# Optimization experiments

Measured on AMD Instinct MI355X. Metric: run time of the kernel, lower is better.

The kernel has to match this reference:

```python
import jax, jax.numpy as jnp
import numpy as np

N = 50000      # nodes
E = 500000     # directed edges
F_IN = 112     # node feature dim
G = 256        # number of graphs in batch


def _lin(key, fan_in, fan_out):
    # torch nn.Linear default init: U(-1/sqrt(fan_in), 1/sqrt(fan_in))
    s = 1.0 / np.sqrt(fan_in)
    kw, kb = jax.random.split(key)
    W = jax.random.uniform(kw, (fan_in, fan_out), jnp.float32, -s, s)
    b = jax.random.uniform(kb, (fan_out,), jnp.float32, -s, s)
    return W, b


def setup_inputs() -> dict:
    key = jax.random.key(0)
    ks = jax.random.split(key, 9)
    x = jax.random.normal(ks[0], (N, F_IN), jnp.float32)
    edge_index = jax.random.randint(ks[1], (2, E), 0, N)
    # sorted graph ids, guaranteeing every graph id 0..G-1 appears
    batch = jnp.sort(jnp.concatenate([jnp.arange(G),
                                      jax.random.randint(ks[2], (N - G,), 0, G)]))
    W1, b1 = _lin(ks[3], F_IN, 336)
    W2, b2 = _lin(ks[4], 336, 168)
    Wg, bg = _lin(ks[5], 168, 84)
    Wf, bf = _lin(ks[6], 84, 42)
    Wo, bo = _lin(ks[7], 42, 1)
    return dict(x=x, edge_index=edge_index, batch=batch,
                W1=W1, b1=b1, W2=W2, b2=b2,
                Wg=Wg, bg=bg, Wf=Wf, bf=bf, Wo=Wo, bo=bo)


def _gcn_conv(x, W, b, src, dst, n):
    """PyG GCNConv: add self-loops, symmetric D^-1/2 A D^-1/2 normalization."""
    h = x @ W                                   # [n, out]
    loop = jnp.arange(n, dtype=src.dtype)
    src_f = jnp.concatenate([src, loop])        # [E+n]
    dst_f = jnp.concatenate([dst, loop])
    deg = jax.ops.segment_sum(jnp.ones(src_f.shape[0], jnp.float32), dst_f, n)
    dinv = jnp.where(deg > 0, jax.lax.rsqrt(deg), 0.0)
    norm = dinv[src_f] * dinv[dst_f]            # [E+n]
    out = jax.ops.segment_sum(h[src_f] * norm[:, None], dst_f, n)
    return out + b


def reference(x, edge_index, batch, W1, b1, W2, b2, Wg, bg, Wf, bf, Wo, bo):
    src, dst = edge_index[0], edge_index[1]
    h = jax.nn.relu(_gcn_conv(x, W1, b1, src, dst, N))
    # dropout is identity in eval mode
    h = jax.nn.relu(_gcn_conv(h, W2, b2, src, dst, N))
    g = jax.ops.segment_max(h, batch, G)        # global max pool -> [G, 168]
    g = jax.nn.relu(g @ Wg + bg)
    g = jax.nn.relu(g @ Wf + bf)
    return g @ Wo + bo                           # [G, 1]
```

## Files before the change

### kernel.cpp

```cpp
#include <hip/hip_runtime.h>
#include <hip/hip_fp16.h>

#define N_NODES 50000
#define MPAD    50048
#define N_EDGES 500000
#define F_IN    112
#define K1P     128
#define F1      336
#define K2P     352
#define F2      168
#define NGRAPH  256
#define SCAN_CHUNK 1024
#define SCAN_BLOCKS ((N_NODES + SCAN_CHUNK - 1) / SCAN_CHUNK)

typedef __attribute__((ext_vector_type(8))) _Float16 f16x8;
typedef __attribute__((ext_vector_type(4))) float f32x4;
typedef unsigned short ushort_t;

__device__ __forceinline__ ushort_t f16_bits(float x) {
    __half h = __float2half_rn(x);
    return *(ushort_t*)&h;
}

__global__ void k_zero_int(int* p, int n) {
    int i = blockIdx.x * blockDim.x + threadIdx.x;
    if (i < n) p[i] = 0;
}
__global__ void k_count_deg(const int* __restrict__ dst, int* __restrict__ dcount, int e2) {
    int i = blockIdx.x * blockDim.x + threadIdx.x;
    if (i < e2) {
        int2 d = ((const int2*)dst)[i];
        atomicAdd(&dcount[d.x], 1);
        atomicAdd(&dcount[d.y], 1);
    }
}

#define CVX_BLOCKS  ((N_NODES * (F_IN / 4) + 255) / 256)
#define CVW1_BLOCKS ((384 * K1P + 255) / 256)
#define CVW2_BLOCKS ((192 * K2P + 255) / 256)
#define RNG_BLOCKS  ((N_NODES + 255) / 256)
#define PREP_BLOCKS (CVX_BLOCKS + CVW1_BLOCKS + CVW2_BLOCKS + RNG_BLOCKS)

__global__ __launch_bounds__(256) void k_prep(const float* __restrict__ x,
                                              const float* __restrict__ W1,
                                              const float* __restrict__ W2,
                                              const int* __restrict__ batch,
                                              ushort_t* __restrict__ x16,
                                              ushort_t* __restrict__ w1t,
                                              ushort_t* __restrict__ w2t,
                                              int* __restrict__ r0, int* __restrict__ r1) {
    int bid = blockIdx.x;
    int t = threadIdx.x;
    if (bid < CVX_BLOCKS) {
        int i = bid * 256 + t;
        if (i < N_NODES * (F_IN / 4)) {
            float4 v = ((const float4*)x)[i];
            __half2 h0 = __floats2half2_rn(v.x, v.y);
            __half2 h1 = __floats2half2_rn(v.z, v.w);
            uint2 u; u.x = *(unsigned*)&h0; u.y = *(unsigned*)&h1;
            ((uint2*)x16)[i] = u;
        }
        return;
    }
    bid -= CVX_BLOCKS;
    if (bid < CVW1_BLOCKS) {
        int idx = bid * 256 + t;
        if (idx < 384 * K1P) {
            int n = idx / K1P, k = idx % K1P;
            float v = (n < F1 && k < F_IN) ? W1[k * F1 + n] : 0.0f;
            w1t[idx] = f16_bits(v);
        }
        return;
    }
    bid -= CVW1_BLOCKS;
    if (bid < CVW2_BLOCKS) {
        int idx = bid * 256 + t;
        if (idx < 192 * K2P) {
            int n = idx / K2P, k = idx % K2P;
            float v = (n < F2 && k < F1) ? W2[k * F2 + n] : 0.0f;
            w2t[idx] = f16_bits(v);
        }
        return;
    }
    bid -= CVW2_BLOCKS;
    {
        int v = bid * 256 + t;
        if (v >= N_NODES) return;
        int b = batch[v];
        if (v == 0 || batch[v - 1] != b) r0[b] = v;
        if (v == N_NODES - 1 || batch[v + 1] != b) r1[b] = v + 1;
    }
}

__global__ __launch_bounds__(SCAN_CHUNK) void k_scan1(const int* __restrict__ dcount,
                                                      int* __restrict__ off,
                                                      int* __restrict__ partials,
                                                      float* __restrict__ dinv, int n) {
    __shared__ int s[SCAN_CHUNK];
    int t = threadIdx.x;
    int i = blockIdx.x * SCAN_CHUNK + t;
    int val = (i < n) ? dcount[i] : 0;
    s[t] = val;
    __syncthreads();
    for (int d = 1; d < SCAN_CHUNK; d <<= 1) {
        int x = (t >= d) ? s[t - d] : 0;
        __syncthreads();
        s[t] += x;
        __syncthreads();
    }
    if (i < n) {
        off[i] = s[t] - val;
        dinv[i] = rsqrtf((float)val + 1.0f);
    }
    if (t == SCAN_CHUNK - 1) partials[blockIdx.x] = s[t];
}
__global__ __launch_bounds__(SCAN_CHUNK) void k_scan3(int* __restrict__ off,
                                                      const int* __restrict__ partials, int n) {
    __shared__ int tmp[SCAN_BLOCKS];
    __shared__ int pref[SCAN_BLOCKS];
    int t = threadIdx.x;
    if (t < SCAN_BLOCKS) tmp[t] = partials[t];
    __syncthreads();
    if (t == 0) {
        int run = 0;
        for (int j = 0; j < SCAN_BLOCKS; ++j) { pref[j] = run; run += tmp[j]; }
    }
    __syncthreads();
    int i = blockIdx.x * SCAN_CHUNK + t;
    if (i < n) off[i] += pref[blockIdx.x];
    if (i == n) off[i] = N_EDGES;
}

__global__ void k_scatter(const int* __restrict__ src, const int* __restrict__ dst,
                          const int* __restrict__ off, int* __restrict__ cur,
                          const float* __restrict__ dinv,
                          int2* __restrict__ csr, int e) {
    int i = blockIdx.x * blockDim.x + threadIdx.x;
    if (i >= e) return;
    int s = src[i], d = dst[i];
    int pos = atomicAdd(&cur[d], 1);
    int2 rec;
    rec.x = s;
    rec.y = __float_as_int(dinv[s] * dinv[d]);
    csr[off[d] + pos] = rec;
}

__global__ __launch_bounds__(256) void k_agg1(const ushort_t* __restrict__ X16,
                                              const int* __restrict__ off,
                                              const int2* __restrict__ csr,
                                              const float* __restrict__ dinv,
                                              ushort_t* __restrict__ aX) {
    int w = (blockIdx.x * 256 + threadIdx.x) >> 6;
    int lane = threadIdx.x & 63;
    if (w >= N_NODES / 2) return;
    const int g = lane >> 5, sl = lane & 31;
    const int v = 2 * w + g;
    const bool act = sl < 28;
    int o0A = off[2 * w], oM = off[2 * w + 1], o1B = off[2 * w + 2];
    int o0 = g ? oM : o0A;
    int n  = g ? (o1B - oM) : (oM - o0A);
    int nmax = max(oM - o0A, o1B - oM);
    float di = dinv[v];
    float4 acc = {0, 0, 0, 0};
    if (act) {
        uint2 u = *(const uint2*)(X16 + (long)v * F_IN + sl * 4);
        float2 f0 = __half22float2(*(__half2*)&u.x);
        float2 f1 = __half22float2(*(__half2*)&u.y);
        float s2 = di * di;
        acc.x = f0.x * s2; acc.y = f0.y * s2; acc.z = f1.x * s2; acc.w = f1.y * s2;
    }
    int nm1 = max(n - 1, 0);
    for (int b = 0; b < nmax; b += 8) {
        int2 e[8];
        #pragma unroll
        for (int j = 0; j < 8; ++j) {
            int cidx = min(o0 + min(b + j, nm1), N_EDGES - 1);
            e[j] = csr[cidx];
        }
        uint2 u[8];
        #pragma unroll
        for (int j = 0; j < 8; ++j) {
            bool valid = (b + j) < n;
            int s = valid ? e[j].x : v;
            if (act) u[j] = *(const uint2*)(X16 + (long)s * F_IN + sl * 4);
        }
        #pragma unroll
        for (int j = 0; j < 8; ++j) {
            bool valid = (b + j) < n;
            float c = valid ? __int_as_float(e[j].y) : 0.0f;
            float2 f0 = __half22float2(*(__half2*)&u[j].x);
            float2 f1 = __half22float2(*(__half2*)&u[j].y);
            acc.x += c * f0.x; acc.y += c * f0.y; acc.z += c * f1.x; acc.w += c * f1.y;
        }
    }
    if (sl < 32) {
        uint2 o = {0, 0};
        if (act) {
            __half2 h0 = __floats2half2_rn(acc.x, acc.y);
            __half2 h1 = __floats2half2_rn(acc.z, acc.w);
            o.x = *(unsigned*)&h0; o.y = *(unsigned*)&h1;
        }
        *(uint2*)(aX + (long)v * K1P + sl * 4) = o;
    }
}

template<int KP, int EPI>
__global__ __launch_bounds__(256) void k_gemm_f16(
        const ushort_t* __restrict__ A, const ushort_t* __restrict__ Bt,
        const float* __restrict__ bias,
        ushort_t* __restrict__ C, int M, int Nreal, int CW) {
    __shared__ ushort_t As[128][40];
    __shared__ ushort_t Bs[64][40];
    const int tid = threadIdx.x;
    const int row0 = blockIdx.y * 128;
    const int col0 = blockIdx.x * 64;
    const int w  = tid >> 6, l = tid & 63;
    const int wm = w >> 1, wn = w & 1;
    const int lm = l & 15, lq = l >> 4;

    f32x4 acc[4][2];
    #pragma unroll
    for (int i = 0; i < 4; ++i)
        #pragma unroll
        for (int j = 0; j < 2; ++j) acc[i][j] = (f32x4){0.f, 0.f, 0.f, 0.f};

    const int arow  = tid >> 2;
    const int akoff = (tid & 3) * 8;

    for (int k0 = 0; k0 < KP; k0 += 32) {
        *(int4*)&As[arow][akoff]      = *(const int4*)&A[(long)(row0 + arow) * KP + k0 + akoff];
        *(int4*)&As[arow + 64][akoff] = *(const int4*)&A[(long)(row0 + arow + 64) * KP + k0 + akoff];
        *(int4*)&Bs[arow][akoff]      = *(const int4*)&Bt[(long)(col0 + arow) * KP + k0 + akoff];
        __syncthreads();

        f16x8 af[4], bf[2];
        #pragma unroll
        for (int ms = 0; ms < 4; ++ms)
            af[ms] = *(const f16x8*)&As[wm * 64 + ms * 16 + lm][lq * 8];
        #pragma unroll
        for (int ns = 0; ns < 2; ++ns)
            bf[ns] = *(const f16x8*)&Bs[wn * 32 + ns * 16 + lm][lq * 8];
        #pragma unroll
        for (int ms = 0; ms < 4; ++ms)
            #pragma unroll
            for (int ns = 0; ns < 2; ++ns)
                acc[ms][ns] = __builtin_amdgcn_mfma_f32_16x16x32_f16(af[ms], bf[ns], acc[ms][ns], 0, 0, 0);
        __syncthreads();
    }

    #pragma unroll
    for (int ms = 0; ms < 4; ++ms) {
        int R = row0 + wm * 64 + ms * 16 + lq * 4;
        #pragma unroll
        for (int ns = 0; ns < 2; ++ns) {
            int col = col0 + wn * 32 + ns * 16 + lm;
            if (EPI == 1) {
                if (col < CW) {
                    float bb = (col < Nreal) ? bias[col] : 0.0f;
                    #pragma unroll
                    for (int i = 0; i < 4; ++i) {
                        int row = R + i;
                        if (row < M) {
                            float r = (col < Nreal) ? fmaxf(acc[ms][ns][i] + bb, 0.0f) : 0.0f;
                            C[(long)row * CW + col] = f16_bits(r);
                        }
                    }
                }
            } else {
                if (col < Nreal) {
                    #pragma unroll
                    for (int i = 0; i < 4; ++i) {
                        int row = R + i;
                        if (row < M) C[(long)row * Nreal + col] = f16_bits(acc[ms][ns][i]);
                    }
                }
            }
        }
    }
}

__global__ __launch_bounds__(256) void k_agg2(const ushort_t* __restrict__ T16,
                                              const int* __restrict__ off,
                                              const int2* __restrict__ csr,
                                              const float* __restrict__ dinv,
                                              const float* __restrict__ b2,
                                              ushort_t* __restrict__ out2) {
    int w = (blockIdx.x * 256 + threadIdx.x) >> 6;
    int lane = threadIdx.x & 63;
    if (w >= N_NODES / 2) return;
    const int g = lane >> 5, sl = lane & 31;
    const int v = 2 * w + g;
    const bool act = sl < 21;
    int o0A = off[2 * w], oM = off[2 * w + 1], o1B = off[2 * w + 2];
    int o0 = g ? oM : o0A;
    int n  = g ? (o1B - oM) : (oM - o0A);
    int nmax = max(oM - o0A, o1B - oM);
    float di = dinv[v];
    float4 a0 = {0, 0, 0, 0}, a1 = {0, 0, 0, 0};
    if (act) {
        uint4 u = *(const uint4*)(T16 + (long)v * F2 + sl * 8);
        float2 f0 = __half22float2(*(__half2*)&u.x);
        float2 f1 = __half22float2(*(__half2*)&u.y);
        float2 f2 = __half22float2(*(__half2*)&u.z);
        float2 f3 = __half22float2(*(__half2*)&u.w);
        float s2 = di * di;
        a0.x = f0.x * s2; a0.y = f0.y * s2; a0.z = f1.x * s2; a0.w = f1.y * s2;
        a1.x = f2.x * s2; a1.y = f2.y * s2; a1.z = f3.x * s2; a1.w = f3.y * s2;
    }
    int nm1 = max(n - 1, 0);
    for (int b = 0; b < nmax; b += 8) {
        int2 e[8];
        #pragma unroll
        for (int j = 0; j < 8; ++j) {
            int cidx = min(o0 + min(b + j, nm1), N_EDGES - 1);
            e[j] = csr[cidx];
        }
        uint4 u[8];
        #pragma unroll
        for (int j = 0; j < 8; ++j) {
            bool valid = (b + j) < n;
            int s = valid ? e[j].x : v;
            if (act) u[j] = *(const uint4*)(T16 + (long)s * F2 + sl * 8);
        }
        #pragma unroll
        for (int j = 0; j < 8; ++j) {
            bool valid = (b + j) < n;
            float c = valid ? __int_as_float(e[j].y) : 0.0f;
            float2 f0 = __half22float2(*(__half2*)&u[j].x);
            float2 f1 = __half22float2(*(__half2*)&u[j].y);
            float2 f2 = __half22float2(*(__half2*)&u[j].z);
            float2 f3 = __half22float2(*(__half2*)&u[j].w);
            a0.x += c * f0.x; a0.y += c * f0.y; a0.z += c * f1.x; a0.w += c * f1.y;
            a1.x += c * f2.x; a1.y += c * f2.y; a1.z += c * f3.x; a1.w += c * f3.y;
        }
    }
    if (act) {
        float4 bb0 = ((const float4*)b2)[sl * 2];
        float4 bb1 = ((const float4*)b2)[sl * 2 + 1];
        __half2 h0 = __floats2half2_rn(fmaxf(a0.x + bb0.x, 0.0f), fmaxf(a0.y + bb0.y, 0.0f));
        __half2 h1 = __floats2half2_rn(fmaxf(a0.z + bb0.z, 0.0f), fmaxf(a0.w + bb0.w, 0.0f));
        __half2 h2 = __floats2half2_rn(fmaxf(a1.x + bb1.x, 0.0f), fmaxf(a1.y + bb1.y, 0.0f));
        __half2 h3 = __floats2half2_rn(fmaxf(a1.z + bb1.z, 0.0f), fmaxf(a1.w + bb1.w, 0.0f));
        uint4 o;
        o.x = *(unsigned*)&h0; o.y = *(unsigned*)&h1;
        o.z = *(unsigned*)&h2; o.w = *(unsigned*)&h3;
        *(uint4*)(out2 + (long)v * F2 + sl * 8) = o;
    }
}

__global__ __launch_bounds__(256) void k_pool_head(const ushort_t* __restrict__ out2,
        const int* __restrict__ r0, const int* __restrict__ r1,
        const float* __restrict__ Wg, const float* __restrict__ bg,
        const float* __restrict__ Wf, const float* __restrict__ bf,
        const float* __restrict__ Wo, const float* __restrict__ bo,
        float* __restrict__ out) {
    __shared__ float4 sm[4][F2 / 4];
    __shared__ float s0[F2];
    __shared__ float s1[84];
    __shared__ float s2[42];
    int gi = blockIdx.x;
    int slot = threadIdx.x >> 6, lane = threadIdx.x & 63;
    int a = r0[gi], b = r1[gi];
    if (lane < F2 / 4) {
        float4 mx = {0, 0, 0, 0};
        for (int v = a + slot; v < b; v += 4) {
            uint2 u = ((const uint2*)(out2 + (long)v * F2))[lane];
            float2 f0 = __half22float2(*(__half2*)&u.x);
            float2 f1 = __half22float2(*(__half2*)&u.y);
            mx.x = fmaxf(mx.x, f0.x); mx.y = fmaxf(mx.y, f0.y);
            mx.z = fmaxf(mx.z, f1.x); mx.w = fmaxf(mx.w, f1.y);
        }
        sm[slot][lane] = mx;
    }
    __syncthreads();
    if (slot == 0 && lane < F2 / 4) {
        float4 m0 = sm[0][lane], m1 = sm[1][lane], m2 = sm[2][lane], m3 = sm[3][lane];
        float4 r;
        r.x = fmaxf(fmaxf(m0.x, m1.x), fmaxf(m2.x, m3.x));
        r.y = fmaxf(fmaxf(m0.y, m1.y), fmaxf(m2.y, m3.y));
        r.z = fmaxf(fmaxf(m0.z, m1.z), fmaxf(m2.z, m3.z));
        r.w = fmaxf(fmaxf(m0.w, m1.w), fmaxf(m2.w, m3.w));
        ((float4*)s0)[lane] = r;
    }
    __syncthreads();
    int t = threadIdx.x;
    if (t < 84) {
        float acc = bg[t];
        #pragma unroll 4
        for (int k = 0; k < F2; ++k) acc += s0[k] * Wg[k * 84 + t];
        s1[t] = fmaxf(acc, 0.0f);
    }
    __syncthreads();
    if (t < 42) {
        float acc = bf[t];
        #pragma unroll 4
        for (int k = 0; k < 84; ++k) acc += s1[k] * Wf[k * 42 + t];
        s2[t] = fmaxf(acc, 0.0f);
    }
    __syncthreads();
    if (t == 0) {
        float acc = bo[0];
        for (int k = 0; k < 42; ++k) acc += s2[k] * Wo[k];
        out[gi] = acc;
    }
}

extern "C" void kernel_launch(void* const* d_in, const int* in_sizes, int n_in,
                              void* d_out, int out_size, void* d_ws, size_t ws_size,
                              hipStream_t stream) {
    const float* x   = (const float*)d_in[0];
    const int*   ei  = (const int*)d_in[1];
    const int*   bat = (const int*)d_in[2];
    const float* W1  = (const float*)d_in[3];
    const float* b1  = (const float*)d_in[4];
    const float* W2  = (const float*)d_in[5];
    const float* b2  = (const float*)d_in[6];
    const float* Wg  = (const float*)d_in[7];
    const float* bg  = (const float*)d_in[8];
    const float* Wf  = (const float*)d_in[9];
    const float* bf  = (const float*)d_in[10];
    const float* Wo  = (const float*)d_in[11];
    const float* bo  = (const float*)d_in[12];
    float* out = (float*)d_out;

    char* p = (char*)d_ws;
    float* dinv     = (float*)p; p += 50048 * 4;
    int*   dcount   = (int*)p;   p += 50048 * 4;
    int*   cur      = (int*)p;   p += 50048 * 4;
    int*   off      = (int*)p;   p += 50064 * 4;
    int*   partials = (int*)p;   p += 64 * 4;
    int*   rng0     = (int*)p;   p += 256 * 4;
    int*   rng1     = (int*)p;   p += 256 * 4;
    int2*  csr      = (int2*)p;  p += (long)N_EDGES * 8;
    ushort_t* x16   = (ushort_t*)p; p += (long)N_NODES * F_IN * 2;
    ushort_t* aX    = (ushort_t*)p; p += (long)MPAD * K1P * 2;
    ushort_t* w1t   = (ushort_t*)p; p += (long)384 * K1P * 2;
    ushort_t* w2t   = (ushort_t*)p; p += (long)192 * K2P * 2;
    ushort_t* h1    = (ushort_t*)p; p += (long)MPAD * K2P * 2;
    ushort_t* t16   = (ushort_t*)p; p += (long)N_NODES * F2 * 2;
    ushort_t* o16   = (ushort_t*)p; p += (long)N_NODES * F2 * 2;

    const int* src = ei;
    const int* dst = ei + N_EDGES;
    const int B = 256;

    k_zero_int<<<(2 * 50048 + B - 1) / B, B, 0, stream>>>(dcount, 2 * 50048);
    k_count_deg<<<(N_EDGES / 2 + B - 1) / B, B, 0, stream>>>(dst, dcount, N_EDGES / 2);
    k_prep<<<PREP_BLOCKS, B, 0, stream>>>(x, W1, W2, bat, x16, w1t, w2t, rng0, rng1);
    k_scan1<<<SCAN_BLOCKS, SCAN_CHUNK, 0, stream>>>(dcount, off, partials, dinv, N_NODES);
    k_scan3<<<SCAN_BLOCKS, SCAN_CHUNK, 0, stream>>>(off, partials, N_NODES);
    k_scatter<<<(N_EDGES + B - 1) / B, B, 0, stream>>>(src, dst, off, cur, dinv, csr, N_EDGES);

    k_agg1<<<(N_NODES / 2 * 64) / 256, 256, 0, stream>>>(x16, off, csr, dinv, aX);
    dim3 gg1(6, MPAD / 128);
    k_gemm_f16<K1P, 1><<<gg1, 256, 0, stream>>>(aX, w1t, b1, h1, N_NODES, F1, K2P);

    dim3 gg2(3, MPAD / 128);
    k_gemm_f16<K2P, 2><<<gg2, 256, 0, stream>>>(h1, w2t, nullptr, t16, N_NODES, F2, 0);
    k_agg2<<<(N_NODES / 2 * 64) / 256, 256, 0, stream>>>(t16, off, csr, dinv, b2, o16);

    k_pool_head<<<NGRAPH, 256, 0, stream>>>(o16, rng0, rng1, Wg, bg, Wf, bf, Wo, bo, out);
}
```

Baseline: 299.4 us.

## Retile GEMMs to wide-N tiles, fold degree count into prep, vectorize scatter

The two GEMM kernels move from 128x64 tiles to 64xNT tiles, with NT=128 for layer 1 and NT=192 for layer 2. The second GEMM then reads each A row once over the whole output width instead of three times. The degree-count kernel is merged into the prep kernel as an extra block range, removing one launch. The scatter kernel now handles two edges per thread with int2 loads. The wider tiles use more accumulators per thread, which may reduce occupancy, and the smaller M tile launches more blocks.

```diff
diff --git a/kernel.cpp b/kernel.cpp
--- a/kernel.cpp
+++ b/kernel.cpp
@@ -26,26 +26,21 @@
     int i = blockIdx.x * blockDim.x + threadIdx.x;
     if (i < n) p[i] = 0;
 }
-__global__ void k_count_deg(const int* __restrict__ dst, int* __restrict__ dcount, int e2) {
-    int i = blockIdx.x * blockDim.x + threadIdx.x;
-    if (i < e2) {
-        int2 d = ((const int2*)dst)[i];
-        atomicAdd(&dcount[d.x], 1);
-        atomicAdd(&dcount[d.y], 1);
-    }
-}
 
 #define CVX_BLOCKS  ((N_NODES * (F_IN / 4) + 255) / 256)
+#define CNT_BLOCKS  ((N_EDGES / 2 + 255) / 256)
 #define CVW1_BLOCKS ((384 * K1P + 255) / 256)
 #define CVW2_BLOCKS ((192 * K2P + 255) / 256)
 #define RNG_BLOCKS  ((N_NODES + 255) / 256)
-#define PREP_BLOCKS (CVX_BLOCKS + CVW1_BLOCKS + CVW2_BLOCKS + RNG_BLOCKS)
+#define PREP_BLOCKS (CVX_BLOCKS + CNT_BLOCKS + CVW1_BLOCKS + CVW2_BLOCKS + RNG_BLOCKS)
 
 __global__ __launch_bounds__(256) void k_prep(const float* __restrict__ x,
+                                              const int* __restrict__ dst,
                                               const float* __restrict__ W1,
                                               const float* __restrict__ W2,
                                               const int* __restrict__ batch,
                                               ushort_t* __restrict__ x16,
+                                              int* __restrict__ dcount,
                                               ushort_t* __restrict__ w1t,
                                               ushort_t* __restrict__ w2t,
                                               int* __restrict__ r0, int* __restrict__ r1) {
@@ -63,6 +58,16 @@
         return;
     }
     bid -= CVX_BLOCKS;
+    if (bid < CNT_BLOCKS) {
+        int i = bid * 256 + t;
+        if (i < N_EDGES / 2) {
+            int2 d = ((const int2*)dst)[i];
+            atomicAdd(&dcount[d.x], 1);
+            atomicAdd(&dcount[d.y], 1);
+        }
+        return;
+    }
+    bid -= CNT_BLOCKS;
     if (bid < CVW1_BLOCKS) {
         int idx = bid * 256 + t;
         if (idx < 384 * K1P) {
@@ -134,15 +139,21 @@
 __global__ void k_scatter(const int* __restrict__ src, const int* __restrict__ dst,
                           const int* __restrict__ off, int* __restrict__ cur,
                           const float* __restrict__ dinv,
-                          int2* __restrict__ csr, int e) {
+                          int2* __restrict__ csr, int e2) {
     int i = blockIdx.x * blockDim.x + threadIdx.x;
-    if (i >= e) return;
-    int s = src[i], d = dst[i];
-    int pos = atomicAdd(&cur[d], 1);
-    int2 rec;
-    rec.x = s;
-    rec.y = __float_as_int(dinv[s] * dinv[d]);
-    csr[off[d] + pos] = rec;
+    if (i >= e2) return;
+    int2 s2 = ((const int2*)src)[i];
+    int2 d2 = ((const int2*)dst)[i];
+    {
+        int pos = atomicAdd(&cur[d2.x], 1);
+        int2 rec; rec.x = s2.x; rec.y = __float_as_int(dinv[s2.x] * dinv[d2.x]);
+        csr[off[d2.x] + pos] = rec;
+    }
+    {
+        int pos = atomicAdd(&cur[d2.y], 1);
+        int2 rec; rec.x = s2.y; rec.y = __float_as_int(dinv[s2.y] * dinv[d2.y]);
+        csr[off[d2.y] + pos] = rec;
+    }
 }
 
 __global__ __launch_bounds__(256) void k_agg1(const ushort_t* __restrict__ X16,
@@ -204,56 +215,59 @@
     }
 }
 
-template<int KP, int EPI>
+template<int NT, int KP, int EPI>
 __global__ __launch_bounds__(256) void k_gemm_f16(
         const ushort_t* __restrict__ A, const ushort_t* __restrict__ Bt,
         const float* __restrict__ bias,
         ushort_t* __restrict__ C, int M, int Nreal, int CW) {
-    __shared__ ushort_t As[128][40];
-    __shared__ ushort_t Bs[64][40];
+    constexpr int NS = NT / 32;
+    __shared__ ushort_t As[64][40];
+    __shared__ ushort_t Bs[NT][40];
     const int tid = threadIdx.x;
-    const int row0 = blockIdx.y * 128;
-    const int col0 = blockIdx.x * 64;
+    const int row0 = blockIdx.y * 64;
+    const int col0 = blockIdx.x * NT;
     const int w  = tid >> 6, l = tid & 63;
     const int wm = w >> 1, wn = w & 1;
     const int lm = l & 15, lq = l >> 4;
 
-    f32x4 acc[4][2];
+    f32x4 acc[2][NS];
     #pragma unroll
-    for (int i = 0; i < 4; ++i)
-        #pragma unroll
-        for (int j = 0; j < 2; ++j) acc[i][j] = (f32x4){0.f, 0.f, 0.f, 0.f};
+    for (int i = 0; i < 2; ++i)
+        #pragma unroll
+        for (int j = 0; j < NS; ++j) acc[i][j] = (f32x4){0.f, 0.f, 0.f, 0.f};
 
     const int arow  = tid >> 2;
     const int akoff = (tid & 3) * 8;
 
     for (int k0 = 0; k0 < KP; k0 += 32) {
-        *(int4*)&As[arow][akoff]      = *(const int4*)&A[(long)(row0 + arow) * KP + k0 + akoff];
-        *(int4*)&As[arow + 64][akoff] = *(const int4*)&A[(long)(row0 + arow + 64) * KP + k0 + akoff];
-        *(int4*)&Bs[arow][akoff]      = *(const int4*)&Bt[(long)(col0 + arow) * KP + k0 + akoff];
+        *(int4*)&As[arow][akoff] = *(const int4*)&A[(long)(row0 + arow) * KP + k0 + akoff];
+        #pragma unroll
+        for (int c = 0; c < NT / 64; ++c)
+            *(int4*)&Bs[c * 64 + arow][akoff] =
+                *(const int4*)&Bt[(long)(col0 + c * 64 + arow) * KP + k0 + akoff];
         __syncthreads();
 
-        f16x8 af[4], bf[2];
-        #pragma unroll
-        for (int ms = 0; ms < 4; ++ms)
-            af[ms] = *(const f16x8*)&As[wm * 64 + ms * 16 + lm][lq * 8];
-        #pragma unroll
-        for (int ns = 0; ns < 2; ++ns)
-            bf[ns] = *(const f16x8*)&Bs[wn * 32 + ns * 16 + lm][lq * 8];
-        #pragma unroll
-        for (int ms = 0; ms < 4; ++ms)
+        f16x8 af[2], bf[NS];
+        #pragma unroll
+        for (int ms = 0; ms < 2; ++ms)
+            af[ms] = *(const f16x8*)&As[wm * 32 + ms * 16 + lm][lq * 8];
+        #pragma unroll
+        for (int ns = 0; ns < NS; ++ns)
+            bf[ns] = *(const f16x8*)&Bs[wn * (NT / 2) + ns * 16 + lm][lq * 8];
+        #pragma unroll
+        for (int ms = 0; ms < 2; ++ms)
             #pragma unroll
-            for (int ns = 0; ns < 2; ++ns)
+            for (int ns = 0; ns < NS; ++ns)
                 acc[ms][ns] = __builtin_amdgcn_mfma_f32_16x16x32_f16(af[ms], bf[ns], acc[ms][ns], 0, 0, 0);
         __syncthreads();
     }
 
     #pragma unroll
-    for (int ms = 0; ms < 4; ++ms) {
-        int R = row0 + wm * 64 + ms * 16 + lq * 4;
-        #pragma unroll
-        for (int ns = 0; ns < 2; ++ns) {
-            int col = col0 + wn * 32 + ns * 16 + lm;
+    for (int ms = 0; ms < 2; ++ms) {
+        int R = row0 + wm * 32 + ms * 16 + lq * 4;
+        #pragma unroll
+        for (int ns = 0; ns < NS; ++ns) {
+            int col = col0 + wn * (NT / 2) + ns * 16 + lm;
             if (EPI == 1) {
                 if (col < CW) {
                     float bb = (col < Nreal) ? bias[col] : 0.0f;
@@ -445,18 +459,17 @@
     const int B = 256;
 
     k_zero_int<<<(2 * 50048 + B - 1) / B, B, 0, stream>>>(dcount, 2 * 50048);
-    k_count_deg<<<(N_EDGES / 2 + B - 1) / B, B, 0, stream>>>(dst, dcount, N_EDGES / 2);
-    k_prep<<<PREP_BLOCKS, B, 0, stream>>>(x, W1, W2, bat, x16, w1t, w2t, rng0, rng1);
+    k_prep<<<PREP_BLOCKS, B, 0, stream>>>(x, dst, W1, W2, bat, x16, dcount, w1t, w2t, rng0, rng1);
     k_scan1<<<SCAN_BLOCKS, SCAN_CHUNK, 0, stream>>>(dcount, off, partials, dinv, N_NODES);
     k_scan3<<<SCAN_BLOCKS, SCAN_CHUNK, 0, stream>>>(off, partials, N_NODES);
-    k_scatter<<<(N_EDGES + B - 1) / B, B, 0, stream>>>(src, dst, off, cur, dinv, csr, N_EDGES);
+    k_scatter<<<(N_EDGES / 2 + B - 1) / B, B, 0, stream>>>(src, dst, off, cur, dinv, csr, N_EDGES / 2);
 
     k_agg1<<<(N_NODES / 2 * 64) / 256, 256, 0, stream>>>(x16, off, csr, dinv, aX);
-    dim3 gg1(6, MPAD / 128);
-    k_gemm_f16<K1P, 1><<<gg1, 256, 0, stream>>>(aX, w1t, b1, h1, N_NODES, F1, K2P);
-
-    dim3 gg2(3, MPAD / 128);
-    k_gemm_f16<K2P, 2><<<gg2, 256, 0, stream>>>(h1, w2t, nullptr, t16, N_NODES, F2, 0);
+    dim3 gg1(3, MPAD / 64);
+    k_gemm_f16<128, K1P, 1><<<gg1, 256, 0, stream>>>(aX, w1t, b1, h1, N_NODES, F1, K2P);
+
+    dim3 gg2(1, MPAD / 64);
+    k_gemm_f16<192, K2P, 2><<<gg2, 256, 0, stream>>>(h1, w2t, nullptr, t16, N_NODES, F2, 0);
     k_agg2<<<(N_NODES / 2 * 64) / 256, 256, 0, stream>>>(t16, off, csr, dinv, b2, o16);
 
     k_pool_head<<<NGRAPH, 256, 0, stream>>>(o16, rng0, rng1, Wg, bg, Wf, bf, Wo, bo, out);
```

Measured after the change: 290.6 us. -3.0%, faster.
